# Kernel optimization log

Hardware: AMD Instinct MI355X
Metric: run time of the kernel (lower is better)

Reference implementation:

```python
import jax, jax.numpy as jnp
import numpy as np

N = 50000
E = 800000
EPS = 1e-12


def sage_conv(x, src, dst, W_l, b_l, W_r):
    # PyG SAGEConv (mean aggr): out = lin_l(mean_{j in N(i)} x_j) + lin_r(x_i)
    msg = x[src]                                             # [E, d] gather
    agg = jax.ops.segment_sum(msg, dst, num_segments=N)      # [N, d]
    cnt = jax.ops.segment_sum(jnp.ones((E,), x.dtype), dst, num_segments=N)
    mean = agg / jnp.maximum(cnt, 1.0)[:, None]              # isolated nodes -> 0
    return mean @ W_l + b_l + x @ W_r


def setup_inputs() -> dict:
    key = jax.random.key(0)
    ks = jax.random.split(key, 12)
    s = 0.05
    return {
        "x": jax.random.normal(ks[0], (N, 128), dtype=jnp.float32),
        "edge_index": jax.random.randint(ks[1], (2, E), 0, N, dtype=jnp.int64),
        # pre: Linear(128 -> 128)
        "pre_W": jax.random.normal(ks[2], (128, 128), dtype=jnp.float32) * s,
        "pre_b": jnp.zeros((128,), dtype=jnp.float32),
        # conv_first: SAGEConv(128 -> 256)
        "W1_l": jax.random.normal(ks[3], (128, 256), dtype=jnp.float32) * s,
        "b1": jnp.zeros((256,), dtype=jnp.float32),
        "W1_r": jax.random.normal(ks[4], (128, 256), dtype=jnp.float32) * s,
        # conv_hidden[0]: SAGEConv(256 -> 256)
        "W2_l": jax.random.normal(ks[5], (256, 256), dtype=jnp.float32) * s,
        "b2": jnp.zeros((256,), dtype=jnp.float32),
        "W2_r": jax.random.normal(ks[6], (256, 256), dtype=jnp.float32) * s,
        # conv_out: SAGEConv(256 -> 256)
        "W3_l": jax.random.normal(ks[7], (256, 256), dtype=jnp.float32) * s,
        "b3": jnp.zeros((256,), dtype=jnp.float32),
        "W3_r": jax.random.normal(ks[8], (256, 256), dtype=jnp.float32) * s,
    }


def reference(x, edge_index, pre_W, pre_b, W1_l, b1, W1_r, W2_l, b2, W2_r, W3_l, b3, W3_r):
    src, dst = edge_index[0], edge_index[1]
    h = x @ pre_W + pre_b                                   # feature_pre Linear
    h = jax.nn.relu(sage_conv(h, src, dst, W1_l, b1, W1_r))  # dropout = identity (eval)
    h = jax.nn.relu(sage_conv(h, src, dst, W2_l, b2, W2_r))
    h = sage_conv(h, src, dst, W3_l, b3, W3_r)
    norm = jnp.sqrt(jnp.sum(h * h, axis=-1, keepdims=True))
    return h / jnp.maximum(norm, EPS)                       # F.normalize(p=2, dim=-1)
```

## Files before the change

kernel.cpp:

```cpp
#include <hip/hip_runtime.h>
#include <cstddef>
#include <cstdint>


typedef __attribute__((ext_vector_type(8))) short short8;
typedef __attribute__((ext_vector_type(4))) float f32x4;

__device__ __forceinline__ unsigned rne_bf16(float f) {
    unsigned b = __float_as_uint(f);
    return (b + 0x7fffu + ((b >> 16) & 1u)) >> 16;
}
__device__ __forceinline__ float bf16_lo(unsigned u) { return __uint_as_float(u << 16); }
__device__ __forceinline__ float bf16_hi(unsigned u) { return __uint_as_float(u & 0xffff0000u); }


__global__ __launch_bounds__(256) void deg_kernel(const int* __restrict__ dst,
                                                  int* __restrict__ deg, int E) {
    int e = blockIdx.x * 256 + threadIdx.x;
    if (e < E) atomicAdd(&deg[dst[e]], 1);
}

__global__ __launch_bounds__(256) void bsum_kernel(const int* __restrict__ deg,
                                                   int* __restrict__ bsum, int n) {
    int i = blockIdx.x * 256 + threadIdx.x;
    int v = (i < n) ? deg[i] : 0;
#pragma unroll
    for (int s = 32; s > 0; s >>= 1) v += __shfl_down(v, s);
    __shared__ int ws[4];
    int lane = threadIdx.x & 63, w = threadIdx.x >> 6;
    if (lane == 0) ws[w] = v;
    __syncthreads();
    if (threadIdx.x == 0) bsum[blockIdx.x] = ws[0] + ws[1] + ws[2] + ws[3];
}

__global__ __launch_bounds__(256) void bscan_kernel(const int* __restrict__ bsum,
                                                    int* __restrict__ boff,
                                                    int* __restrict__ off,
                                                    int nb, int n, int E) {
    int t = threadIdx.x;
    int v = (t < nb) ? bsum[t] : 0;
    int incl = v;
#pragma unroll
    for (int s = 1; s < 64; s <<= 1) {
        int u = __shfl_up(incl, s);
        if ((t & 63) >= s) incl += u;
    }
    __shared__ int ws[4];
    int lane = t & 63, w = t >> 6;
    if (lane == 63) ws[w] = incl;
    __syncthreads();
    int woff = 0;
    for (int j = 0; j < w; ++j) woff += ws[j];
    if (t < nb) boff[t] = woff + incl - v;
    if (t == 0) off[n] = E;
}

__global__ __launch_bounds__(256) void scan_kernel(const int* __restrict__ deg,
                                                   const int* __restrict__ boff,
                                                   int* __restrict__ off,
                                                   float* __restrict__ inv, int n) {
    int i = blockIdx.x * 256 + threadIdx.x;
    int v = (i < n) ? deg[i] : 0;
    int incl = v;
#pragma unroll
    for (int s = 1; s < 64; s <<= 1) {
        int u = __shfl_up(incl, s);
        if ((threadIdx.x & 63) >= s) incl += u;
    }
    __shared__ int ws[4];
    int lane = threadIdx.x & 63, w = threadIdx.x >> 6;
    if (lane == 63) ws[w] = incl;
    __syncthreads();
    int woff = 0;
    for (int j = 0; j < w; ++j) woff += ws[j];
    if (i < n) {
        off[i] = boff[blockIdx.x] + woff + incl - v;
        inv[i] = 1.0f / fmaxf((float)v, 1.0f);
    }
}

__global__ __launch_bounds__(256) void fill_kernel(const int* __restrict__ src,
                                                   const int* __restrict__ dst,
                                                   const int* __restrict__ off,
                                                   int* __restrict__ deg,
                                                   int* __restrict__ ssrc, int E) {
    int e = blockIdx.x * 256 + threadIdx.x;
    if (e >= E) return;
    int d = dst[e];
    int pos = off[d] + atomicSub(&deg[d], 1) - 1;
    ssrc[pos] = src[e];
}


__global__ __launch_bounds__(256) void xconv(const float* __restrict__ x,
                                             uint2* __restrict__ xb, int n4) {
    int i = blockIdx.x * 256 + threadIdx.x;
    if (i >= n4) return;
    float4 v = ((const float4*)x)[i];
    uint2 o;
    o.x = rne_bf16(v.x) | (rne_bf16(v.y) << 16);
    o.y = rne_bf16(v.z) | (rne_bf16(v.w) << 16);
    xb[i] = o;
}

__global__ __launch_bounds__(256) void wprep(
    const float* __restrict__ pre_W, const float* __restrict__ W1_l,
    const float* __restrict__ W1_r, const float* __restrict__ W2_l,
    const float* __restrict__ W2_r, const float* __restrict__ W3_l,
    const float* __restrict__ W3_r,
    unsigned short* __restrict__ WT0, unsigned short* __restrict__ WT1,
    unsigned short* __restrict__ WT2, unsigned short* __restrict__ WT3,
    unsigned short* __restrict__ WT4, unsigned short* __restrict__ WT5,
    unsigned short* __restrict__ WT6) {
    int idx = blockIdx.x * 256 + threadIdx.x;
    if (idx < 16384) {
        int k = idx >> 7, n = idx & 127;
        WT0[n * 128 + k] = (unsigned short)rne_bf16(pre_W[idx]);
        return;
    }
    idx -= 16384;
    if (idx < 32768) {
        int k = idx >> 8, n = idx & 255;
        WT1[n * 128 + k] = (unsigned short)rne_bf16(W1_l[idx]);
        return;
    }
    idx -= 32768;
    if (idx < 32768) {
        int k = idx >> 8, n = idx & 255;
        WT2[n * 128 + k] = (unsigned short)rne_bf16(W1_r[idx]);
        return;
    }
    idx -= 32768;
    if (idx < 65536) {
        int k = idx >> 8, n = idx & 255;
        WT3[n * 256 + k] = (unsigned short)rne_bf16(W2_l[idx]);
        return;
    }
    idx -= 65536;
    if (idx < 65536) {
        int k = idx >> 8, n = idx & 255;
        WT4[n * 256 + k] = (unsigned short)rne_bf16(W2_r[idx]);
        return;
    }
    idx -= 65536;
    if (idx < 65536) {
        int k = idx >> 8, n = idx & 255;
        WT5[n * 256 + k] = (unsigned short)rne_bf16(W3_l[idx]);
        return;
    }
    idx -= 65536;
    if (idx < 65536) {
        int k = idx >> 8, n = idx & 255;
        WT6[n * 256 + k] = (unsigned short)rne_bf16(W3_r[idx]);
    }
}


template <int D>
__global__ __launch_bounds__(256) void gather_b(const unsigned short* __restrict__ h,
                                                const int* __restrict__ off,
                                                const int* __restrict__ ssrc,
                                                const float* __restrict__ inv,
                                                unsigned short* __restrict__ agg, int n) {
    int node = blockIdx.x * 4 + (threadIdx.x >> 6);
    if (node >= n) return;
    int lane = threadIdx.x & 63;
    int beg = off[node], end = off[node + 1];
    float sc = inv[node];

    if (D == 256) {
        const unsigned short* col = h + (lane << 2);
        float a0 = 0, a1 = 0, a2 = 0, a3 = 0;
        float b0 = 0, b1 = 0, b2 = 0, b3 = 0;
        int k = beg;
        for (; k + 1 < end; k += 2) {
            int s0 = ssrc[k], s1 = ssrc[k + 1];
            uint2 u = *(const uint2*)(col + (size_t)s0 * 256);
            uint2 v = *(const uint2*)(col + (size_t)s1 * 256);
            a0 += bf16_lo(u.x); a1 += bf16_hi(u.x);
            a2 += bf16_lo(u.y); a3 += bf16_hi(u.y);
            b0 += bf16_lo(v.x); b1 += bf16_hi(v.x);
            b2 += bf16_lo(v.y); b3 += bf16_hi(v.y);
        }
        if (k < end) {
            uint2 u = *(const uint2*)(col + (size_t)ssrc[k] * 256);
            a0 += bf16_lo(u.x); a1 += bf16_hi(u.x);
            a2 += bf16_lo(u.y); a3 += bf16_hi(u.y);
        }
        a0 = (a0 + b0) * sc; a1 = (a1 + b1) * sc;
        a2 = (a2 + b2) * sc; a3 = (a3 + b3) * sc;
        uint2 o;
        o.x = rne_bf16(a0) | (rne_bf16(a1) << 16);
        o.y = rne_bf16(a2) | (rne_bf16(a3) << 16);
        *(uint2*)(agg + (size_t)node * 256 + (lane << 2)) = o;
    } else {
        const unsigned short* col = h + (lane << 1);
        float a0 = 0, a1 = 0, b0 = 0, b1 = 0;
        int k = beg;
        for (; k + 1 < end; k += 2) {
            int s0 = ssrc[k], s1 = ssrc[k + 1];
            unsigned u = *(const unsigned*)(col + (size_t)s0 * 128);
            unsigned v = *(const unsigned*)(col + (size_t)s1 * 128);
            a0 += bf16_lo(u); a1 += bf16_hi(u);
            b0 += bf16_lo(v); b1 += bf16_hi(v);
        }
        if (k < end) {
            unsigned u = *(const unsigned*)(col + (size_t)ssrc[k] * 128);
            a0 += bf16_lo(u); a1 += bf16_hi(u);
        }
        a0 = (a0 + b0) * sc; a1 = (a1 + b1) * sc;
        *(unsigned*)(agg + (size_t)node * 128 + (lane << 1)) =
            rne_bf16(a0) | (rne_bf16(a1) << 16);
    }
}

__global__ __launch_bounds__(256) void gemm_bt(
    const unsigned short* __restrict__ A1, const unsigned short* __restrict__ W1T,
    const unsigned short* __restrict__ A2, const unsigned short* __restrict__ W2T,
    const float* __restrict__ bias,
    unsigned short* __restrict__ outb, float* __restrict__ outf,
    int M, int K, int Nn, int relu) {
    __shared__ __align__(16) unsigned short As[128 * 64];
    __shared__ __align__(16) unsigned short Bs[128 * 64];

    const int t = threadIdx.x;
    const int lane = t & 63;
    const int w = t >> 6;
    const int wm = w >> 1, wn = w & 1;
    const int m0 = blockIdx.x * 128;
    const int n0 = blockIdx.y * 128;

    f32x4 acc[4][4];
#pragma unroll
    for (int i = 0; i < 4; ++i)
#pragma unroll
        for (int j = 0; j < 4; ++j) acc[i][j] = (f32x4){0.f, 0.f, 0.f, 0.f};

    for (int pass = 0; pass < 2; ++pass) {
        const unsigned short* A = pass ? A2 : A1;
        const unsigned short* W = pass ? W2T : W1T;
        if (pass && A2 == nullptr) break;

        for (int k0 = 0; k0 < K; k0 += 64) {
#pragma unroll
            for (int r = 0; r < 4; ++r) {
                int p = r * 256 + t;
                int row = p >> 3, slot = p & 7;
                int c = slot ^ (row & 7);
                int gm = m0 + row;
                if (gm >= M) gm = M - 1;
                uint4 va = *(const uint4*)(A + (size_t)gm * K + k0 + c * 8);
                uint4 vb = *(const uint4*)(W + (size_t)(n0 + row) * K + k0 + c * 8);
                *(uint4*)&As[(size_t)p * 8] = va;
                *(uint4*)&Bs[(size_t)p * 8] = vb;
            }
            __syncthreads();
#pragma unroll
            for (int kk = 0; kk < 2; ++kk) {
                short8 af[4], bfr[4];
                int ac = kk * 4 + (lane >> 4);
#pragma unroll
                for (int i = 0; i < 4; ++i) {
                    int arow = wm * 64 + i * 16 + (lane & 15);
                    af[i] = *(const short8*)&As[arow * 64 + ((ac ^ (arow & 7)) << 3)];
                    int brow = wn * 64 + i * 16 + (lane & 15);
                    bfr[i] = *(const short8*)&Bs[brow * 64 + ((ac ^ (brow & 7)) << 3)];
                }
#pragma unroll
                for (int mi = 0; mi < 4; ++mi)
#pragma unroll
                    for (int ni = 0; ni < 4; ++ni)
                        acc[mi][ni] = __builtin_amdgcn_mfma_f32_16x16x32_bf16(
                            af[mi], bfr[ni], acc[mi][ni], 0, 0, 0);
            }
            __syncthreads();
        }
    }

#pragma unroll
    for (int ni = 0; ni < 4; ++ni) {
        int n = n0 + wn * 64 + ni * 16 + (lane & 15);
        float bv = (bias != nullptr) ? bias[n] : 0.0f;
#pragma unroll
        for (int mi = 0; mi < 4; ++mi) {
            int mbase = m0 + wm * 64 + mi * 16 + ((lane >> 4) << 2);
#pragma unroll
            for (int r = 0; r < 4; ++r) {
                int m = mbase + r;
                if (m >= M) continue;
                float v = acc[mi][ni][r] + bv;
                if (relu) v = fmaxf(v, 0.0f);
                if (outb) outb[(size_t)m * Nn + n] = (unsigned short)rne_bf16(v);
                else      outf[(size_t)m * Nn + n] = v;
            }
        }
    }
}

__global__ __launch_bounds__(256) void norm_kernel(float* __restrict__ out, int M) {
    int row  = blockIdx.x * 4 + (threadIdx.x >> 6);
    int lane = threadIdx.x & 63;
    if (row >= M) return;
    float4 v = *(float4*)(out + (size_t)row * 256 + (lane << 2));
    float s = v.x * v.x + v.y * v.y + v.z * v.z + v.w * v.w;
#pragma unroll
    for (int off = 32; off > 0; off >>= 1) s += __shfl_down(s, off);
    s = __shfl(s, 0);
    float scale = 1.0f / fmaxf(sqrtf(s), 1e-12f);
    v.x *= scale; v.y *= scale; v.z *= scale; v.w *= scale;
    *(float4*)(out + (size_t)row * 256 + (lane << 2)) = v;
}

extern "C" void kernel_launch(void* const* d_in, const int* in_sizes, int n_in,
                              void* d_out, int out_size, void* d_ws, size_t ws_size,
                              hipStream_t stream) {
    const int N = 50000;
    const int E = 800000;
    const int NB = (N + 255) / 256;

    const float* x     = (const float*)d_in[0];
    const int*   ei    = (const int*)d_in[1];
    const float* pre_W = (const float*)d_in[2];
    const float* pre_b = (const float*)d_in[3];
    const float* W1_l  = (const float*)d_in[4];
    const float* b1    = (const float*)d_in[5];
    const float* W1_r  = (const float*)d_in[6];
    const float* W2_l  = (const float*)d_in[7];
    const float* b2    = (const float*)d_in[8];
    const float* W2_r  = (const float*)d_in[9];
    const float* W3_l  = (const float*)d_in[10];
    const float* b3    = (const float*)d_in[11];
    const float* W3_r  = (const float*)d_in[12];
    float* out = (float*)d_out;

    const int* src = ei;
    const int* dst = ei + E;

    int* deg  = (int*)d_ws;
    int* off  = deg + N;
    int* bsum = off + N + 1;
    int* boff = bsum + 256;
    int* ssrc = boff + 256;
    size_t int_words = (size_t)2 * N + 1 + 512 + E;
    int_words = (int_words + 3) & ~(size_t)3;

    float* inv = (float*)d_ws + int_words;
    unsigned short* us = (unsigned short*)(inv + N);

    unsigned short* xb  = us;                 us += (size_t)N * 128;
    unsigned short* WT0 = us;                 us += 16384;
    unsigned short* WT1 = us;                 us += 32768;
    unsigned short* WT2 = us;                 us += 32768;
    unsigned short* WT3 = us;                 us += 65536;
    unsigned short* WT4 = us;                 us += 65536;
    unsigned short* WT5 = us;                 us += 65536;
    unsigned short* WT6 = us;                 us += 65536;
    unsigned short* h0b   = us;               us += (size_t)N * 128;
    unsigned short* agg1b = us;               us += (size_t)N * 128;
    unsigned short* h1b   = us;               us += (size_t)N * 256;
    unsigned short* agg2b = us;               us += (size_t)N * 256;
    unsigned short* h2b   = us;               us += (size_t)N * 256;
    unsigned short* agg3b = us;               us += (size_t)N * 256;

    hipMemsetAsync(deg, 0, (size_t)N * sizeof(int), stream);
    deg_kernel<<<(E + 255) / 256, 256, 0, stream>>>(dst, deg, E);
    bsum_kernel<<<NB, 256, 0, stream>>>(deg, bsum, N);
    bscan_kernel<<<1, 256, 0, stream>>>(bsum, boff, off, NB, N, E);
    scan_kernel<<<NB, 256, 0, stream>>>(deg, boff, off, inv, N);
    fill_kernel<<<(E + 255) / 256, 256, 0, stream>>>(src, dst, off, deg, ssrc, E);

    xconv<<<(N * 128 / 4 + 255) / 256, 256, 0, stream>>>(x, (uint2*)xb, N * 128 / 4);
    wprep<<<(344064 + 255) / 256, 256, 0, stream>>>(pre_W, W1_l, W1_r, W2_l, W2_r,
                                                    W3_l, W3_r, WT0, WT1, WT2, WT3,
                                                    WT4, WT5, WT6);

    const int MT = (N + 127) / 128;
    const int AG = (N + 3) / 4;

    gemm_bt<<<dim3(MT, 1), 256, 0, stream>>>(xb, WT0, nullptr, nullptr, pre_b,
                                             h0b, nullptr, N, 128, 128, 0);

    gather_b<128><<<AG, 256, 0, stream>>>(h0b, off, ssrc, inv, agg1b, N);
    gemm_bt<<<dim3(MT, 2), 256, 0, stream>>>(agg1b, WT1, h0b, WT2, b1,
                                             h1b, nullptr, N, 128, 256, 1);

    gather_b<256><<<AG, 256, 0, stream>>>(h1b, off, ssrc, inv, agg2b, N);
    gemm_bt<<<dim3(MT, 2), 256, 0, stream>>>(agg2b, WT3, h1b, WT4, b2,
                                             h2b, nullptr, N, 256, 256, 1);

    gather_b<256><<<AG, 256, 0, stream>>>(h2b, off, ssrc, inv, agg3b, N);
    gemm_bt<<<dim3(MT, 2), 256, 0, stream>>>(agg3b, WT5, h2b, WT6, b3,
                                             nullptr, out, N, 256, 256, 0);

    norm_kernel<<<AG, 256, 0, stream>>>(out, N);
}
```

Baseline: 548.4 us.

## Split neighbor gather into feature slices with 16-bit sorted source indices

The CSR source index array is stored as 16-bit values, which fit because N is below 65536, halving index traffic. The gather kernel changes from one wavefront per node to four lanes per node, 16 nodes per wavefront. Each block handles a 32-column feature slice, and each lane does 16-byte row loads, giving more independent memory requests in flight. In exchange, lanes in a wavefront diverge on differing node degrees, and each index is re-read once per feature slice. Partial 64-byte row segments may also waste cache-line bandwidth.

```diff
diff --git a/kernel.cpp b/kernel.cpp
--- a/kernel.cpp
+++ b/kernel.cpp
@@ -83,12 +83,13 @@
                                                    const int* __restrict__ dst,
                                                    const int* __restrict__ off,
                                                    int* __restrict__ deg,
-                                                   int* __restrict__ ssrc, int E) {
+                                                   unsigned short* __restrict__ ssrc16,
+                                                   int E) {
     int e = blockIdx.x * 256 + threadIdx.x;
     if (e >= E) return;
     int d = dst[e];
     int pos = off[d] + atomicSub(&deg[d], 1) - 1;
-    ssrc[pos] = src[e];
+    ssrc16[pos] = (unsigned short)src[e];
 }
 
 
@@ -157,61 +158,55 @@
 
 
 template <int D>
-__global__ __launch_bounds__(256) void gather_b(const unsigned short* __restrict__ h,
+__global__ __launch_bounds__(256) void gather_s(const unsigned short* __restrict__ h,
                                                 const int* __restrict__ off,
-                                                const int* __restrict__ ssrc,
+                                                const unsigned short* __restrict__ ssrc16,
                                                 const float* __restrict__ inv,
                                                 unsigned short* __restrict__ agg, int n) {
-    int node = blockIdx.x * 4 + (threadIdx.x >> 6);
+    constexpr int NS = D / 32;
+    const int s    = blockIdx.x & (NS - 1);
+    const int g    = blockIdx.x / NS;
+    const int lane = threadIdx.x & 63;
+    const int node = g * 64 + ((threadIdx.x >> 6) << 4) + (lane >> 2);
     if (node >= n) return;
-    int lane = threadIdx.x & 63;
-    int beg = off[node], end = off[node + 1];
-    float sc = inv[node];
-
-    if (D == 256) {
-        const unsigned short* col = h + (lane << 2);
-        float a0 = 0, a1 = 0, a2 = 0, a3 = 0;
-        float b0 = 0, b1 = 0, b2 = 0, b3 = 0;
-        int k = beg;
-        for (; k + 1 < end; k += 2) {
-            int s0 = ssrc[k], s1 = ssrc[k + 1];
-            uint2 u = *(const uint2*)(col + (size_t)s0 * 256);
-            uint2 v = *(const uint2*)(col + (size_t)s1 * 256);
-            a0 += bf16_lo(u.x); a1 += bf16_hi(u.x);
-            a2 += bf16_lo(u.y); a3 += bf16_hi(u.y);
-            b0 += bf16_lo(v.x); b1 += bf16_hi(v.x);
-            b2 += bf16_lo(v.y); b3 += bf16_hi(v.y);
-        }
-        if (k < end) {
-            uint2 u = *(const uint2*)(col + (size_t)ssrc[k] * 256);
-            a0 += bf16_lo(u.x); a1 += bf16_hi(u.x);
-            a2 += bf16_lo(u.y); a3 += bf16_hi(u.y);
-        }
-        a0 = (a0 + b0) * sc; a1 = (a1 + b1) * sc;
-        a2 = (a2 + b2) * sc; a3 = (a3 + b3) * sc;
-        uint2 o;
-        o.x = rne_bf16(a0) | (rne_bf16(a1) << 16);
-        o.y = rne_bf16(a2) | (rne_bf16(a3) << 16);
-        *(uint2*)(agg + (size_t)node * 256 + (lane << 2)) = o;
-    } else {
-        const unsigned short* col = h + (lane << 1);
-        float a0 = 0, a1 = 0, b0 = 0, b1 = 0;
-        int k = beg;
-        for (; k + 1 < end; k += 2) {
-            int s0 = ssrc[k], s1 = ssrc[k + 1];
-            unsigned u = *(const unsigned*)(col + (size_t)s0 * 128);
-            unsigned v = *(const unsigned*)(col + (size_t)s1 * 128);
-            a0 += bf16_lo(u); a1 += bf16_hi(u);
-            b0 += bf16_lo(v); b1 += bf16_hi(v);
-        }
-        if (k < end) {
-            unsigned u = *(const unsigned*)(col + (size_t)ssrc[k] * 128);
-            a0 += bf16_lo(u); a1 += bf16_hi(u);
-        }
-        a0 = (a0 + b0) * sc; a1 = (a1 + b1) * sc;
-        *(unsigned*)(agg + (size_t)node * 128 + (lane << 1)) =
-            rne_bf16(a0) | (rne_bf16(a1) << 16);
-    }
+    const int sub = lane & 3;
+    const int beg = off[node], end = off[node + 1];
+    const float sc = inv[node];
+    const unsigned short* col = h + s * 32 + (sub << 3);
+
+    float a[8] = {0, 0, 0, 0, 0, 0, 0, 0};
+    float b[8] = {0, 0, 0, 0, 0, 0, 0, 0};
+    int k = beg;
+    for (; k + 1 < end; k += 2) {
+        unsigned s0 = __builtin_nontemporal_load(&ssrc16[k]);
+        unsigned s1 = __builtin_nontemporal_load(&ssrc16[k + 1]);
+        uint4 u = *(const uint4*)(col + (size_t)s0 * D);
+        uint4 v = *(const uint4*)(col + (size_t)s1 * D);
+        a[0] += bf16_lo(u.x); a[1] += bf16_hi(u.x);
+        a[2] += bf16_lo(u.y); a[3] += bf16_hi(u.y);
+        a[4] += bf16_lo(u.z); a[5] += bf16_hi(u.z);
+        a[6] += bf16_lo(u.w); a[7] += bf16_hi(u.w);
+        b[0] += bf16_lo(v.x); b[1] += bf16_hi(v.x);
+        b[2] += bf16_lo(v.y); b[3] += bf16_hi(v.y);
+        b[4] += bf16_lo(v.z); b[5] += bf16_hi(v.z);
+        b[6] += bf16_lo(v.w); b[7] += bf16_hi(v.w);
+    }
+    if (k < end) {
+        unsigned s0 = __builtin_nontemporal_load(&ssrc16[k]);
+        uint4 u = *(const uint4*)(col + (size_t)s0 * D);
+        a[0] += bf16_lo(u.x); a[1] += bf16_hi(u.x);
+        a[2] += bf16_lo(u.y); a[3] += bf16_hi(u.y);
+        a[4] += bf16_lo(u.z); a[5] += bf16_hi(u.z);
+        a[6] += bf16_lo(u.w); a[7] += bf16_hi(u.w);
+    }
+#pragma unroll
+    for (int i = 0; i < 8; ++i) a[i] = (a[i] + b[i]) * sc;
+    uint4 o;
+    o.x = rne_bf16(a[0]) | (rne_bf16(a[1]) << 16);
+    o.y = rne_bf16(a[2]) | (rne_bf16(a[3]) << 16);
+    o.z = rne_bf16(a[4]) | (rne_bf16(a[5]) << 16);
+    o.w = rne_bf16(a[6]) | (rne_bf16(a[7]) << 16);
+    *(uint4*)(agg + (size_t)node * D + s * 32 + (sub << 3)) = o;
 }
 
 __global__ __launch_bounds__(256) void gemm_bt(
@@ -340,8 +335,8 @@
     int* off  = deg + N;
     int* bsum = off + N + 1;
     int* boff = bsum + 256;
-    int* ssrc = boff + 256;
-    size_t int_words = (size_t)2 * N + 1 + 512 + E;
+    unsigned short* ssrc16 = (unsigned short*)(boff + 256);
+    size_t int_words = (size_t)2 * N + 1 + 512 + E / 2;
     int_words = (int_words + 3) & ~(size_t)3;
 
     float* inv = (float*)d_ws + int_words;
@@ -367,7 +362,7 @@
     bsum_kernel<<<NB, 256, 0, stream>>>(deg, bsum, N);
     bscan_kernel<<<1, 256, 0, stream>>>(bsum, boff, off, NB, N, E);
     scan_kernel<<<NB, 256, 0, stream>>>(deg, boff, off, inv, N);
-    fill_kernel<<<(E + 255) / 256, 256, 0, stream>>>(src, dst, off, deg, ssrc, E);
+    fill_kernel<<<(E + 255) / 256, 256, 0, stream>>>(src, dst, off, deg, ssrc16, E);
 
     xconv<<<(N * 128 / 4 + 255) / 256, 256, 0, stream>>>(x, (uint2*)xb, N * 128 / 4);
     wprep<<<(344064 + 255) / 256, 256, 0, stream>>>(pre_W, W1_l, W1_r, W2_l, W2_r,
@@ -376,19 +371,20 @@
 
     const int MT = (N + 127) / 128;
     const int AG = (N + 3) / 4;
+    const int GG = (N + 63) / 64;
 
     gemm_bt<<<dim3(MT, 1), 256, 0, stream>>>(xb, WT0, nullptr, nullptr, pre_b,
                                              h0b, nullptr, N, 128, 128, 0);
 
-    gather_b<128><<<AG, 256, 0, stream>>>(h0b, off, ssrc, inv, agg1b, N);
+    gather_s<128><<<GG * 4, 256, 0, stream>>>(h0b, off, ssrc16, inv, agg1b, N);
     gemm_bt<<<dim3(MT, 2), 256, 0, stream>>>(agg1b, WT1, h0b, WT2, b1,
                                              h1b, nullptr, N, 128, 256, 1);
 
-    gather_b<256><<<AG, 256, 0, stream>>>(h1b, off, ssrc, inv, agg2b, N);
+    gather_s<256><<<GG * 8, 256, 0, stream>>>(h1b, off, ssrc16, inv, agg2b, N);
     gemm_bt<<<dim3(MT, 2), 256, 0, stream>>>(agg2b, WT3, h1b, WT4, b2,
                                              h2b, nullptr, N, 256, 256, 1);
 
-    gather_b<256><<<AG, 256, 0, stream>>>(h2b, off, ssrc, inv, agg3b, N);
+    gather_s<256><<<GG * 8, 256, 0, stream>>>(h2b, off, ssrc16, inv, agg3b, N);
     gemm_bt<<<dim3(MT, 2), 256, 0, stream>>>(agg3b, WT5, h2b, WT6, b3,
                                              nullptr, out, N, 256, 256, 0);
 
```

New measurement: 761.8 us. 1.39x slower.
